# Optimization experiments

Measured on AMD Instinct MI355X. Metric: run time of the kernel, lower is better.

## Reference

```python
import jax, jax.numpy as jnp
import numpy as np

C = 32        # latent_channels
BCH = 6       # bottleneck_channels
H, W = 180, 320
N = H * W
B = 32


def _hilbert_walk(h, w):
    """Faithful port of FlattenDeflatten._hilbert_curve: Morton/Z-order bit
    interleave over (i, j), stable-sorted by key (ties broken by raster index).
    Returns flat raster indices in walk order."""
    i = np.arange(h, dtype=np.int64)[:, None]
    j = np.arange(w, dtype=np.int64)[None, :]
    z = np.zeros((h, w), dtype=np.int64)
    for bit in range(16):
        z |= ((i >> bit) & 1) << (2 * bit + 1)
        z |= ((j >> bit) & 1) << (2 * bit)
    # coords.sort() on (z, flat_idx) == stable argsort of z over raster order
    return np.argsort(z.ravel(), kind='stable')


def setup_inputs() -> dict:
    key = jax.random.key(0)
    ks = jax.random.split(key, 6)
    walk = _hilbert_walk(H, W)
    unwalk = np.zeros_like(walk)
    unwalk[walk] = np.arange(N)
    # torch Conv1d default init: U(-1/sqrt(fan_in), 1/sqrt(fan_in)), kernel=1
    bf = 1.0 / np.sqrt(C)
    bd = 1.0 / np.sqrt(BCH)
    return {
        "latent": jax.random.normal(ks[0], (B, C, H, W), dtype=jnp.float32),
        "w_flat": jax.random.uniform(ks[1], (BCH, C), jnp.float32, -bf, bf),
        "b_flat": jax.random.uniform(ks[2], (BCH,), jnp.float32, -bf, bf),
        "w_deflat": jax.random.uniform(ks[3], (C, BCH), jnp.float32, -bd, bd),
        "b_deflat": jax.random.uniform(ks[4], (C,), jnp.float32, -bd, bd),
        "spatial_embed": jax.random.normal(ks[5], (1, C, N), dtype=jnp.float32) * 0.02,
        "walk_idx": jnp.asarray(walk, dtype=jnp.int32),
        "unwalk_idx": jnp.asarray(unwalk, dtype=jnp.int32),
    }


def reference(latent, w_flat, b_flat, w_deflat, b_deflat, spatial_embed,
              walk_idx, unwalk_idx):
    Bb, Cc, Hh, Ww = latent.shape
    # flatten: serialize along walk order, then 1x1 conv (channel GEMM)
    seq = latent.reshape(Bb, Cc, Hh * Ww)[:, :, walk_idx]          # (B, C, N)
    flat = jnp.einsum('oc,bcn->bon', w_flat, seq) + b_flat[:, None]  # (B, BCH, N)
    # deflatten: 1x1 conv back, add positional embed, inverse permutation
    dseq = (jnp.einsum('co,bon->bcn', w_deflat, flat)
            + b_deflat[:, None] + spatial_embed)                    # (B, C, N)
    recon = dseq[:, :, unwalk_idx].reshape(Bb, Cc, Hh, Ww)
    return (recon, flat)
```

## Files before the change

### kernel.cpp

```cpp
#include <hip/hip_runtime.h>

#define CCH 32
#define BCH 6
#define HH  180
#define WW  320
#define NN  (HH*WW)
#define BATCH 32
#define RPC 4
#define CHUNKS (HH/RPC)
#define THREADS 320

typedef float f32x2 __attribute__((ext_vector_type(2)));
typedef float f32x4 __attribute__((ext_vector_type(4)));

__global__ __launch_bounds__(256) void permute_se(
    const float* __restrict__ se, const int* __restrict__ unwalk,
    float* __restrict__ se_r)
{
    const int p = blockIdx.x * 256 + threadIdx.x;
    const int n = unwalk[p];
    #pragma unroll 8
    for (int c = 0; c < CCH; ++c)
        se_r[(size_t)c * NN + p] = se[(size_t)c * NN + n];
}

template<int SE_RASTER>
__global__ __launch_bounds__(THREADS) void fused_flatten_deflatten(
    const float* __restrict__ latent,
    const float* __restrict__ w_flat,
    const float* __restrict__ b_flat,
    const float* __restrict__ w_deflat,
    const float* __restrict__ b_deflat,
    const float* __restrict__ se,
    const int*   __restrict__ unwalk,
    float* __restrict__ recon,
    float* __restrict__ flat_out)
{
    __shared__ float s_wf[BCH*CCH];
    __shared__ float s_wd[CCH*BCH];
    __shared__ float s_bf[BCH];
    __shared__ float s_bd[CCH];

    const int t  = threadIdx.x;
    const int bx = blockIdx.x;
    const int r  = bx >> 5;
    const int b  = bx & 31;

    if (t < BCH*CCH) { s_wf[t] = w_flat[t]; s_wd[t] = w_deflat[t]; }
    if (t < BCH)     s_bf[t] = b_flat[t];
    if (t < CCH)     s_bd[t] = b_deflat[t];
    __syncthreads();

    const int i  = RPC*r + t/80;
    const int j  = 4*(t%80);
    const int p  = i*WW + j;

    const int nb = unwalk[(i & ~1)*WW + j];
    const int n2 = nb + 2*(i & 1);

    const float* latb   = latent + (size_t)b * (CCH*NN) + p;
    float*       reconb = recon  + (size_t)b * (CCH*NN) + p;

    float acc[BCH][4];
    #pragma unroll
    for (int o = 0; o < BCH; ++o) {
        const float bo = s_bf[o];
        acc[o][0] = bo; acc[o][1] = bo; acc[o][2] = bo; acc[o][3] = bo;
    }

    #pragma unroll 8
    for (int c = 0; c < CCH; ++c) {
        const f32x4 x = __builtin_nontemporal_load(
            reinterpret_cast<const f32x4*>(latb + (size_t)c*NN));
        #pragma unroll
        for (int o = 0; o < BCH; ++o) {
            const float w = s_wf[o*CCH + c];
            acc[o][0] += w*x.x; acc[o][1] += w*x.y;
            acc[o][2] += w*x.z; acc[o][3] += w*x.w;
        }
    }

    float* fb = flat_out + (size_t)b * (BCH*NN) + n2;
    #pragma unroll
    for (int o = 0; o < BCH; ++o) {
        f32x2 lo; lo.x = acc[o][0]; lo.y = acc[o][1];
        f32x2 hi; hi.x = acc[o][2]; hi.y = acc[o][3];
        *reinterpret_cast<f32x2*>(fb + (size_t)o*NN)     = lo;
        *reinterpret_cast<f32x2*>(fb + (size_t)o*NN + 4) = hi;
    }

    #pragma unroll 8
    for (int c = 0; c < CCH; ++c) {
        float s0, s1, s2, s3;
        if (SE_RASTER) {
            const f32x4 s4 = *reinterpret_cast<const f32x4*>(se + (size_t)c*NN + p);
            s0 = s4.x; s1 = s4.y; s2 = s4.z; s3 = s4.w;
        } else {
            const f32x2 a = *reinterpret_cast<const f32x2*>(se + (size_t)c*NN + n2);
            const f32x2 bq = *reinterpret_cast<const f32x2*>(se + (size_t)c*NN + n2 + 4);
            s0 = a.x; s1 = a.y; s2 = bq.x; s3 = bq.y;
        }
        const float bd = s_bd[c];
        float y0 = bd + s0, y1 = bd + s1, y2 = bd + s2, y3 = bd + s3;
        #pragma unroll
        for (int o = 0; o < BCH; ++o) {
            const float w = s_wd[c*BCH + o];
            y0 += w*acc[o][0]; y1 += w*acc[o][1];
            y2 += w*acc[o][2]; y3 += w*acc[o][3];
        }
        f32x4 yv; yv.x = y0; yv.y = y1; yv.z = y2; yv.w = y3;
        *reinterpret_cast<f32x4*>(reconb + (size_t)c*NN) = yv;
    }
}

extern "C" void kernel_launch(void* const* d_in, const int* in_sizes, int n_in,
                              void* d_out, int out_size, void* d_ws, size_t ws_size,
                              hipStream_t stream) {
    const float* latent   = (const float*)d_in[0];
    const float* w_flat   = (const float*)d_in[1];
    const float* b_flat   = (const float*)d_in[2];
    const float* w_deflat = (const float*)d_in[3];
    const float* b_deflat = (const float*)d_in[4];
    const float* se       = (const float*)d_in[5];
    const int*   unwalk   = (const int*)d_in[7];

    float* recon = (float*)d_out;
    float* flat  = (float*)d_out + (size_t)BATCH * CCH * NN;

    const size_t se_bytes = (size_t)CCH * NN * sizeof(float);
    dim3 grid(CHUNKS * BATCH);
    dim3 block(THREADS);

    if (ws_size >= se_bytes) {
        float* se_r = (float*)d_ws;
        permute_se<<<dim3(NN/256), dim3(256), 0, stream>>>(se, unwalk, se_r);
        fused_flatten_deflatten<1><<<grid, block, 0, stream>>>(
            latent, w_flat, b_flat, w_deflat, b_deflat, se_r, unwalk, recon, flat);
    } else {
        fused_flatten_deflatten<0><<<grid, block, 0, stream>>>(
            latent, w_flat, b_flat, w_deflat, b_deflat, se, unwalk, recon, flat);
    }
}
```

Measured before the change: 131.7 us.

## Vectorize SE permute with folded bias, nontemporal recon stores, larger blocks

```diff
diff --git a/kernel.cpp b/kernel.cpp
--- a/kernel.cpp
+++ b/kernel.cpp
@@ -6,22 +6,31 @@
 #define WW  320
 #define NN  (HH*WW)
 #define BATCH 32
-#define RPC 4
-#define CHUNKS (HH/RPC)
-#define THREADS 320
+#define RPC 8
+#define CHUNKS ((HH + RPC - 1)/RPC)
+#define THREADS 640
 
 typedef float f32x2 __attribute__((ext_vector_type(2)));
 typedef float f32x4 __attribute__((ext_vector_type(4)));
 
 __global__ __launch_bounds__(256) void permute_se(
     const float* __restrict__ se, const int* __restrict__ unwalk,
-    float* __restrict__ se_r)
+    const float* __restrict__ b_deflat, float* __restrict__ se_r)
 {
-    const int p = blockIdx.x * 256 + threadIdx.x;
-    const int n = unwalk[p];
+    const int p = (blockIdx.x * 256 + threadIdx.x) * 4;
+    if (p >= NN) return;
+    const int i  = p / WW;
+    const int j  = p % WW;
+    const int nb = unwalk[(i & ~1)*WW + j];
+    const int n2 = nb + 2*(i & 1);
     #pragma unroll 8
-    for (int c = 0; c < CCH; ++c)
-        se_r[(size_t)c * NN + p] = se[(size_t)c * NN + n];
+    for (int c = 0; c < CCH; ++c) {
+        const f32x2 a  = *reinterpret_cast<const f32x2*>(se + (size_t)c*NN + n2);
+        const f32x2 b2 = *reinterpret_cast<const f32x2*>(se + (size_t)c*NN + n2 + 4);
+        const float bd = b_deflat[c];
+        f32x4 v; v.x = a.x + bd; v.y = a.y + bd; v.z = b2.x + bd; v.w = b2.y + bd;
+        *reinterpret_cast<f32x4*>(se_r + (size_t)c*NN + p) = v;
+    }
 }
 
 template<int SE_RASTER>
@@ -52,6 +61,7 @@
     __syncthreads();
 
     const int i  = RPC*r + t/80;
+    if (i >= HH) return;
     const int j  = 4*(t%80);
     const int p  = i*WW + j;
 
@@ -91,17 +101,16 @@
 
     #pragma unroll 8
     for (int c = 0; c < CCH; ++c) {
-        float s0, s1, s2, s3;
+        float y0, y1, y2, y3;
         if (SE_RASTER) {
             const f32x4 s4 = *reinterpret_cast<const f32x4*>(se + (size_t)c*NN + p);
-            s0 = s4.x; s1 = s4.y; s2 = s4.z; s3 = s4.w;
+            y0 = s4.x; y1 = s4.y; y2 = s4.z; y3 = s4.w;
         } else {
-            const f32x2 a = *reinterpret_cast<const f32x2*>(se + (size_t)c*NN + n2);
+            const f32x2 a  = *reinterpret_cast<const f32x2*>(se + (size_t)c*NN + n2);
             const f32x2 bq = *reinterpret_cast<const f32x2*>(se + (size_t)c*NN + n2 + 4);
-            s0 = a.x; s1 = a.y; s2 = bq.x; s3 = bq.y;
+            const float bd = s_bd[c];
+            y0 = bd + a.x; y1 = bd + a.y; y2 = bd + bq.x; y3 = bd + bq.y;
         }
-        const float bd = s_bd[c];
-        float y0 = bd + s0, y1 = bd + s1, y2 = bd + s2, y3 = bd + s3;
         #pragma unroll
         for (int o = 0; o < BCH; ++o) {
             const float w = s_wd[c*BCH + o];
@@ -109,7 +118,8 @@
             y2 += w*acc[o][2]; y3 += w*acc[o][3];
         }
         f32x4 yv; yv.x = y0; yv.y = y1; yv.z = y2; yv.w = y3;
-        *reinterpret_cast<f32x4*>(reconb + (size_t)c*NN) = yv;
+        __builtin_nontemporal_store(yv,
+            reinterpret_cast<f32x4*>(reconb + (size_t)c*NN));
     }
 }
 
@@ -133,7 +143,8 @@
 
     if (ws_size >= se_bytes) {
         float* se_r = (float*)d_ws;
-        permute_se<<<dim3(NN/256), dim3(256), 0, stream>>>(se, unwalk, se_r);
+        permute_se<<<dim3((NN/4 + 255)/256), dim3(256), 0, stream>>>(
+            se, unwalk, b_deflat, se_r);
         fused_flatten_deflatten<1><<<grid, block, 0, stream>>>(
             latent, w_flat, b_flat, w_deflat, b_deflat, se_r, unwalk, recon, flat);
     } else {
```

After: 131.7 us. Within noise of the previous version (+0.0%).
